# Performance work log

Hardware: AMD Instinct MI355X
Metric: run time of the kernel (lower is better)

The kernel has to match this reference:

```python
import jax, jax.numpy as jnp
import numpy as np

N, C, D, K = 8192, 1024, 256, 20
N_WAYS = 20
REC_OUT = 7 * 7 * 256  # 12544

def _lrelu(v):
    return jnp.where(v > 0, v, 0.01 * v)  # nn.LeakyReLU default slope

def setup_inputs() -> dict:
    key = jax.random.key(0)
    ks = jax.random.split(key, 16)
    s = lambda shape, k, scale: (jax.random.normal(ks[k], shape, jnp.float32) * scale)
    inp = {
        "x": jax.random.normal(ks[0], (N, C), jnp.float32),
        "prototypes": jax.random.normal(ks[1], (K, D), jnp.float32),
        # sigmas in (0.1, 0.5) as in SigmaScheduler(sigma_min=0.1, sigma_max=0.5)
        "sigmas": 0.1 + 0.4 * jax.random.uniform(ks[2], (K,), jnp.float32),
        "prior": jax.random.uniform(ks[3], (K,), jnp.float32) + 1e-3,
        "W1c": s((C, C), 4, C ** -0.5), "b1c": jnp.zeros((C,), jnp.float32),
        "W2c": s((C, D), 5, C ** -0.5), "b2c": jnp.zeros((D,), jnp.float32),
        "W1b": s((C, C), 6, C ** -0.5), "b1b": jnp.zeros((C,), jnp.float32),
        "W2b": s((C, 4 * (N_WAYS + 1)), 7, C ** -0.5), "b2b": jnp.zeros((4 * (N_WAYS + 1),), jnp.float32),
        "Wr1": s((D, 512), 8, D ** -0.5), "br1": jnp.zeros((512,), jnp.float32),
        "Wr2": s((512, REC_OUT), 9, 512 ** -0.5), "br2": jnp.zeros((REC_OUT,), jnp.float32),
    }
    return inp

def reference(x, prototypes, sigmas, prior,
              W1c, b1c, W2c, b2c,
              W1b, b1b, W2b, b2b,
              Wr1, br1, Wr2, br2):
    # cls_score MLP -> embeddings, L2-normalized
    emb = _lrelu(x @ W1c + b1c) @ W2c + b2c                      # [N, D]
    emb = emb / jnp.linalg.norm(emb, axis=-1, keepdims=True)
    bbox_deltas = _lrelu(x @ W1b + b1b) @ W2b + b2b              # [N, 4*(n_ways+1)]
    # prototypes are unit-normed (randn_normed)
    P = prototypes / jnp.linalg.norm(prototypes, axis=-1, keepdims=True)  # [K, D]
    # squared euclidean distance via dot products (avoids N x K x D intermediate)
    d2 = (jnp.sum(emb * emb, axis=-1, keepdims=True)
          + jnp.sum(P * P, axis=-1)[None, :]
          - 2.0 * (emb @ P.T))                                   # [N, K]
    proba = jnp.exp(-d2 / 2.0 / (sigmas[None, :] ** 2))          # [N, K]
    # priors: softmax(prior / prior.max())
    priors = jax.nn.softmax(prior / jnp.max(prior))
    proba = proba * priors[None, :]
    proba_bg = 1.0 - jnp.max(proba, axis=-1, keepdims=True)      # [N, 1]
    scores = jnp.concatenate([proba_bg, proba], axis=-1)         # [N, K+1]
    # reconstruction MLP
    reconstructions = _lrelu(emb @ Wr1 + br1) @ Wr2 + br2        # [N, 12544]
    return scores, bbox_deltas, emb, reconstructions
```

## Files before the change

### kernel.cpp

```cpp
#include <hip/hip_runtime.h>
#include <hip/hip_bf16.h>

typedef __attribute__((ext_vector_type(8))) __bf16 bf16x8;
typedef __attribute__((ext_vector_type(4))) float f32x4;
typedef __hip_bfloat16 bf16t;

#define DEV __device__ __forceinline__

DEV void async16(const void* g, void* l) {
    __builtin_amdgcn_global_load_lds(
        (const __attribute__((address_space(1))) unsigned int*)g,
        (__attribute__((address_space(3))) unsigned int*)l,
        16, 0, 0);
}

DEV float wave_sum(float s) {
#pragma unroll
    for (int o = 32; o > 0; o >>= 1) s += __shfl_xor(s, o);
    return s;
}

DEV float wave_max(float s) {
#pragma unroll
    for (int o = 32; o > 0; o >>= 1) s = fmaxf(s, __shfl_xor(s, o));
    return s;
}

__global__ void cast_bf16_kernel(const float* __restrict__ in, bf16t* __restrict__ out, int n4) {
    int i = blockIdx.x * blockDim.x + threadIdx.x;
    if (i >= n4) return;
    f32x4 v = *(const f32x4*)(in + (size_t)i * 4);
    bf16t* o = out + (size_t)i * 4;
    o[0] = __float2bfloat16(v.x);
    o[1] = __float2bfloat16(v.y);
    o[2] = __float2bfloat16(v.z);
    o[3] = __float2bfloat16(v.w);
}

__global__ void transpose_bf16_kernel(const float* __restrict__ in, bf16t* __restrict__ out,
                                      int R, int Ccols, int RP) {
    int idx = blockIdx.x * blockDim.x + threadIdx.x;
    if (idx >= RP * R) return;
    int n = idx / R;
    int k = idx - n * R;
    float v = (n < Ccols) ? in[(size_t)k * Ccols + n] : 0.0f;
    out[idx] = __float2bfloat16(v);
}

template <bool LRELU, bool OUTF32, bool NGUARD>
__global__ __launch_bounds__(256) void gemm_bt(
    const bf16t* __restrict__ A, const bf16t* __restrict__ BT,
    const float* __restrict__ bias,
    float* __restrict__ Cf, bf16t* __restrict__ Cb,
    int M, int N, int K) {
    __shared__ __align__(16) char ldsA[8192];
    __shared__ __align__(16) char ldsB[8192];

    const int tid = threadIdx.x;
    const int lane = tid & 63;
    const int w = tid >> 6;
    const int wr = w >> 1, wc = w & 1;
    const int brow = blockIdx.y * 128;
    const int bcol = blockIdx.x * 128;

    f32x4 acc[4][4] = {};

    const int q0 = tid, q1 = tid + 256;
    const int r0 = q0 >> 2, c0 = q0 & 3;
    const int r1 = q1 >> 2, c1 = q1 & 3;
    const int ka0 = ((c0 ^ ((r0 >> 1) & 3)) << 3);
    const int ka1 = ((c1 ^ ((r1 >> 1) & 3)) << 3);

    const bf16t* aSrc0 = A + (size_t)(brow + r0) * K + ka0;
    const bf16t* aSrc1 = A + (size_t)(brow + r1) * K + ka1;
    const bf16t* bSrc0 = BT + (size_t)(bcol + r0) * K + ka0;
    const bf16t* bSrc1 = BT + (size_t)(bcol + r1) * K + ka1;
    char* ldA0 = ldsA + w * 1024;
    char* ldA1 = ldsA + 4096 + w * 1024;
    char* ldB0 = ldsB + w * 1024;
    char* ldB1 = ldsB + 4096 + w * 1024;

    const int j = lane >> 4, rl = lane & 15;
    const char* aAddr[4];
    const char* bAddr[4];
#pragma unroll
    for (int mi = 0; mi < 4; ++mi) {
        int row = wr * 64 + mi * 16 + rl;
        aAddr[mi] = ldsA + row * 64 + ((j ^ ((row >> 1) & 3)) << 4);
    }
#pragma unroll
    for (int ni = 0; ni < 4; ++ni) {
        int row = wc * 64 + ni * 16 + rl;
        bAddr[ni] = ldsB + row * 64 + ((j ^ ((row >> 1) & 3)) << 4);
    }

    for (int k0 = 0; k0 < K; k0 += 32) {
        __syncthreads();
        async16(aSrc0 + k0, ldA0);
        async16(aSrc1 + k0, ldA1);
        async16(bSrc0 + k0, ldB0);
        async16(bSrc1 + k0, ldB1);
        __syncthreads();

        bf16x8 af[4], bfr[4];
#pragma unroll
        for (int mi = 0; mi < 4; ++mi) af[mi] = *(const bf16x8*)aAddr[mi];
#pragma unroll
        for (int ni = 0; ni < 4; ++ni) bfr[ni] = *(const bf16x8*)bAddr[ni];
#pragma unroll
        for (int mi = 0; mi < 4; ++mi)
#pragma unroll
            for (int ni = 0; ni < 4; ++ni)
                acc[mi][ni] = __builtin_amdgcn_mfma_f32_16x16x32_bf16(af[mi], bfr[ni], acc[mi][ni], 0, 0, 0);
    }

#pragma unroll
    for (int mi = 0; mi < 4; ++mi) {
#pragma unroll
        for (int ni = 0; ni < 4; ++ni) {
            int col = bcol + wc * 64 + ni * 16 + (lane & 15);
            if (!NGUARD || col < N) {
                float bv = bias[col];
#pragma unroll
                for (int r = 0; r < 4; ++r) {
                    int row = brow + wr * 64 + mi * 16 + (lane >> 4) * 4 + r;
                    float v = acc[mi][ni][r] + bv;
                    if (LRELU) v = v > 0.0f ? v : 0.01f * v;
                    if (OUTF32) Cf[(size_t)row * N + col] = v;
                    else        Cb[(size_t)row * N + col] = __float2bfloat16(v);
                }
            }
        }
    }
}

__global__ void normalize_kernel(const float* __restrict__ raw, float* __restrict__ outf,
                                 bf16t* __restrict__ outb) {
    int row = blockIdx.x * 4 + (threadIdx.x >> 6);
    int lane = threadIdx.x & 63;
    f32x4 v = *(const f32x4*)(raw + (size_t)row * 256 + lane * 4);
    float s = wave_sum(v.x * v.x + v.y * v.y + v.z * v.z + v.w * v.w);
    float rn = 1.0f / sqrtf(s);
    f32x4 o = v * rn;
    *(f32x4*)(outf + (size_t)row * 256 + lane * 4) = o;
    bf16t* ob = outb + (size_t)row * 256 + lane * 4;
    ob[0] = __float2bfloat16(o.x);
    ob[1] = __float2bfloat16(o.y);
    ob[2] = __float2bfloat16(o.z);
    ob[3] = __float2bfloat16(o.w);
}

__global__ void proto_kernel(const float* __restrict__ proto, const float* __restrict__ prior,
                             float* __restrict__ Pn, float* __restrict__ sp, float* __restrict__ priors) {
    int w = threadIdx.x >> 6, lane = threadIdx.x & 63;
    for (int r = w; r < 20; r += 4) {
        f32x4 v = *(const f32x4*)(proto + (size_t)r * 256 + lane * 4);
        float s = wave_sum(v.x * v.x + v.y * v.y + v.z * v.z + v.w * v.w);
        float rn = 1.0f / sqrtf(s);
        f32x4 p = v * rn;
        *(f32x4*)(Pn + (size_t)r * 256 + lane * 4) = p;
        float s2 = wave_sum(p.x * p.x + p.y * p.y + p.z * p.z + p.w * p.w);
        if (lane == 0) sp[r] = s2;
    }
    if (threadIdx.x < 64) {
        float pv = (lane < 20) ? prior[lane] : -1e30f;
        float m = wave_max(pv);
        float e = (lane < 20) ? expf(pv / m) : 0.0f;
        float ssum = wave_sum(e);
        if (lane < 20) priors[lane] = e / ssum;
    }
}

__global__ void scores_kernel(const float* __restrict__ emb, const float* __restrict__ Pn,
                              const float* __restrict__ sp, const float* __restrict__ priors,
                              const float* __restrict__ sig, float* __restrict__ out) {
    int row = blockIdx.x * 4 + (threadIdx.x >> 6);
    int lane = threadIdx.x & 63;
    f32x4 e = *(const f32x4*)(emb + (size_t)row * 256 + lane * 4);
    float se = wave_sum(e.x * e.x + e.y * e.y + e.z * e.z + e.w * e.w);
    float keep = 0.0f, mx = -1.0f;
    for (int k = 0; k < 20; ++k) {
        f32x4 p = *(const f32x4*)(Pn + (size_t)k * 256 + lane * 4);
        float d = wave_sum(e.x * p.x + e.y * p.y + e.z * p.z + e.w * p.w);
        float d2 = se + sp[k] - 2.0f * d;
        float sgv = sig[k];
        float pr = expf(-d2 / (2.0f * sgv * sgv)) * priors[k];
        mx = fmaxf(mx, pr);
        if (lane == k + 1) keep = pr;
    }
    if (lane == 0) keep = 1.0f - mx;
    if (lane < 21) out[(size_t)row * 21 + lane] = keep;
}

extern "C" void kernel_launch(void* const* d_in, const int* in_sizes, int n_in,
                              void* d_out, int out_size, void* d_ws, size_t ws_size,
                              hipStream_t stream) {
    const float* x     = (const float*)d_in[0];
    const float* proto = (const float*)d_in[1];
    const float* sig   = (const float*)d_in[2];
    const float* prior = (const float*)d_in[3];
    const float* W1c = (const float*)d_in[4];
    const float* b1c = (const float*)d_in[5];
    const float* W2c = (const float*)d_in[6];
    const float* b2c = (const float*)d_in[7];
    const float* W1b = (const float*)d_in[8];
    const float* b1b = (const float*)d_in[9];
    const float* W2b = (const float*)d_in[10];
    const float* b2b = (const float*)d_in[11];
    const float* Wr1 = (const float*)d_in[12];
    const float* br1 = (const float*)d_in[13];
    const float* Wr2 = (const float*)d_in[14];
    const float* br2 = (const float*)d_in[15];

    float* out = (float*)d_out;
    float* out_scores = out;
    float* out_bbox   = out + 172032;
    float* out_emb    = out + 860160;
    float* out_rec    = out + 2957312;

    char* ws = (char*)d_ws;
    size_t off = 0;
    auto alloc = [&](size_t b) { char* p = ws + off; off += (b + 255) & ~(size_t)255; return p; };
    bf16t* xb     = (bf16t*)alloc(8192ull * 1024 * 2);
    bf16t* w1ct   = (bf16t*)alloc(1024ull * 1024 * 2);
    bf16t* w1bt   = (bf16t*)alloc(1024ull * 1024 * 2);
    bf16t* w2ct   = (bf16t*)alloc(256ull * 1024 * 2);
    bf16t* w2bt   = (bf16t*)alloc(128ull * 1024 * 2);
    bf16t* wr1t   = (bf16t*)alloc(512ull * 256 * 2);
    bf16t* wr2t   = (bf16t*)alloc(12544ull * 512 * 2);
    bf16t* hc     = (bf16t*)alloc(8192ull * 1024 * 2);
    bf16t* hb     = (bf16t*)alloc(8192ull * 1024 * 2);
    float* embraw = (float*)alloc(8192ull * 256 * 4);
    bf16t* embb   = (bf16t*)alloc(8192ull * 256 * 2);
    bf16t* rech   = (bf16t*)alloc(8192ull * 512 * 2);
    float* Pn     = (float*)alloc(20 * 256 * 4);
    float* spv    = (float*)alloc(20 * 4);
    float* priors = (float*)alloc(20 * 4);
    (void)ws_size; (void)in_sizes; (void)n_in; (void)out_size;

    cast_bf16_kernel<<<8192, 256, 0, stream>>>(x, xb, 8192 * 1024 / 4);
    transpose_bf16_kernel<<<4096, 256, 0, stream>>>(W1c, w1ct, 1024, 1024, 1024);
    transpose_bf16_kernel<<<4096, 256, 0, stream>>>(W1b, w1bt, 1024, 1024, 1024);
    transpose_bf16_kernel<<<1024, 256, 0, stream>>>(W2c, w2ct, 1024, 256, 256);
    transpose_bf16_kernel<<<512, 256, 0, stream>>>(W2b, w2bt, 1024, 84, 128);
    transpose_bf16_kernel<<<512, 256, 0, stream>>>(Wr1, wr1t, 256, 512, 512);
    transpose_bf16_kernel<<<25088, 256, 0, stream>>>(Wr2, wr2t, 512, 12544, 12544);

    gemm_bt<true, false, false><<<dim3(8, 64), 256, 0, stream>>>(xb, w1ct, b1c, nullptr, hc, 8192, 1024, 1024);
    gemm_bt<true, false, false><<<dim3(8, 64), 256, 0, stream>>>(xb, w1bt, b1b, nullptr, hb, 8192, 1024, 1024);
    gemm_bt<false, true, false><<<dim3(2, 64), 256, 0, stream>>>(hc, w2ct, b2c, embraw, nullptr, 8192, 256, 1024);
    gemm_bt<false, true, true><<<dim3(1, 64), 256, 0, stream>>>(hb, w2bt, b2b, out_bbox, nullptr, 8192, 84, 1024);
    normalize_kernel<<<2048, 256, 0, stream>>>(embraw, out_emb, embb);
    proto_kernel<<<1, 256, 0, stream>>>(proto, prior, Pn, spv, priors);
    scores_kernel<<<2048, 256, 0, stream>>>(out_emb, Pn, spv, priors, sig, out_scores);
    gemm_bt<true, false, false><<<dim3(4, 64), 256, 0, stream>>>(embb, wr1t, br1, nullptr, rech, 8192, 512, 256);
    gemm_bt<false, true, false><<<dim3(98, 64), 256, 0, stream>>>(rech, wr2t, br2, out_rec, nullptr, 8192, 12544, 512);
}
```

Baseline: 802.9 us.

## Tile weight transposes, fuse first-layer GEMMs, merge normalize with scores

Replaces the naive strided transpose with a 32x32 LDS-tiled transpose so weight reads and writes are coalesced. Both first-layer GEMMs are merged into one 8192x2048 GEMM with a split bias, and the second-layer GEMMs read their half through a leading-dimension stride. The normalize and scores kernels are fused, and the cast kernel now writes 16-byte vectors. Together these cut launch count and redundant memory traffic, at the cost of extra lda and bias-select arguments in the GEMM.

```diff
diff --git a/kernel.cpp b/kernel.cpp
--- a/kernel.cpp
+++ b/kernel.cpp
@@ -26,31 +26,46 @@
     return s;
 }
 
-__global__ void cast_bf16_kernel(const float* __restrict__ in, bf16t* __restrict__ out, int n4) {
+__global__ void cast_bf16_kernel(const float* __restrict__ in, bf16t* __restrict__ out, int n8) {
     int i = blockIdx.x * blockDim.x + threadIdx.x;
-    if (i >= n4) return;
-    f32x4 v = *(const f32x4*)(in + (size_t)i * 4);
-    bf16t* o = out + (size_t)i * 4;
-    o[0] = __float2bfloat16(v.x);
-    o[1] = __float2bfloat16(v.y);
-    o[2] = __float2bfloat16(v.z);
-    o[3] = __float2bfloat16(v.w);
-}
-
-__global__ void transpose_bf16_kernel(const float* __restrict__ in, bf16t* __restrict__ out,
-                                      int R, int Ccols, int RP) {
-    int idx = blockIdx.x * blockDim.x + threadIdx.x;
-    if (idx >= RP * R) return;
-    int n = idx / R;
-    int k = idx - n * R;
-    float v = (n < Ccols) ? in[(size_t)k * Ccols + n] : 0.0f;
-    out[idx] = __float2bfloat16(v);
+    if (i >= n8) return;
+    f32x4 a = *(const f32x4*)(in + (size_t)i * 8);
+    f32x4 b = *(const f32x4*)(in + (size_t)i * 8 + 4);
+    union { bf16t h[8]; uint4 u; } r;
+    r.h[0] = __float2bfloat16(a.x); r.h[1] = __float2bfloat16(a.y);
+    r.h[2] = __float2bfloat16(a.z); r.h[3] = __float2bfloat16(a.w);
+    r.h[4] = __float2bfloat16(b.x); r.h[5] = __float2bfloat16(b.y);
+    r.h[6] = __float2bfloat16(b.z); r.h[7] = __float2bfloat16(b.w);
+    *(uint4*)(out + (size_t)i * 8) = r.u;
+}
+
+__global__ void transpose_tile_kernel(const float* __restrict__ in, bf16t* __restrict__ out,
+                                      int R, int C, int CP) {
+    __shared__ float tile[32][33];
+    const int nt = blockIdx.x * 32;
+    const int kt = blockIdx.y * 32;
+    const int tx = threadIdx.x & 31;
+    const int ty = threadIdx.x >> 5;
+#pragma unroll
+    for (int i = 0; i < 4; ++i) {
+        int k = kt + ty + i * 8;
+        int n = nt + tx;
+        tile[ty + i * 8][tx] = (k < R && n < C) ? in[(size_t)k * C + n] : 0.0f;
+    }
+    __syncthreads();
+#pragma unroll
+    for (int i = 0; i < 4; ++i) {
+        int n = nt + ty + i * 8;
+        int k = kt + tx;
+        if (n < CP && k < R)
+            out[(size_t)n * R + k] = __float2bfloat16(tile[tx][ty + i * 8]);
+    }
 }
 
 template <bool LRELU, bool OUTF32, bool NGUARD>
 __global__ __launch_bounds__(256) void gemm_bt(
-    const bf16t* __restrict__ A, const bf16t* __restrict__ BT,
-    const float* __restrict__ bias,
+    const bf16t* __restrict__ A, int lda, const bf16t* __restrict__ BT,
+    const float* __restrict__ bias0, const float* __restrict__ bias1, int nsplit,
     float* __restrict__ Cf, bf16t* __restrict__ Cb,
     int M, int N, int K) {
     __shared__ __align__(16) char ldsA[8192];
@@ -71,8 +86,8 @@
     const int ka0 = ((c0 ^ ((r0 >> 1) & 3)) << 3);
     const int ka1 = ((c1 ^ ((r1 >> 1) & 3)) << 3);
 
-    const bf16t* aSrc0 = A + (size_t)(brow + r0) * K + ka0;
-    const bf16t* aSrc1 = A + (size_t)(brow + r1) * K + ka1;
+    const bf16t* aSrc0 = A + (size_t)(brow + r0) * lda + ka0;
+    const bf16t* aSrc1 = A + (size_t)(brow + r1) * lda + ka1;
     const bf16t* bSrc0 = BT + (size_t)(bcol + r0) * K + ka0;
     const bf16t* bSrc1 = BT + (size_t)(bcol + r1) * K + ka1;
     char* ldA0 = ldsA + w * 1024;
@@ -120,7 +135,7 @@
         for (int ni = 0; ni < 4; ++ni) {
             int col = bcol + wc * 64 + ni * 16 + (lane & 15);
             if (!NGUARD || col < N) {
-                float bv = bias[col];
+                float bv = (col < nsplit) ? bias0[col] : bias1[col - nsplit];
 #pragma unroll
                 for (int r = 0; r < 4; ++r) {
                     int row = brow + wr * 64 + mi * 16 + (lane >> 4) * 4 + r;
@@ -132,22 +147,6 @@
             }
         }
     }
-}
-
-__global__ void normalize_kernel(const float* __restrict__ raw, float* __restrict__ outf,
-                                 bf16t* __restrict__ outb) {
-    int row = blockIdx.x * 4 + (threadIdx.x >> 6);
-    int lane = threadIdx.x & 63;
-    f32x4 v = *(const f32x4*)(raw + (size_t)row * 256 + lane * 4);
-    float s = wave_sum(v.x * v.x + v.y * v.y + v.z * v.z + v.w * v.w);
-    float rn = 1.0f / sqrtf(s);
-    f32x4 o = v * rn;
-    *(f32x4*)(outf + (size_t)row * 256 + lane * 4) = o;
-    bf16t* ob = outb + (size_t)row * 256 + lane * 4;
-    ob[0] = __float2bfloat16(o.x);
-    ob[1] = __float2bfloat16(o.y);
-    ob[2] = __float2bfloat16(o.z);
-    ob[3] = __float2bfloat16(o.w);
 }
 
 __global__ void proto_kernel(const float* __restrict__ proto, const float* __restrict__ prior,
@@ -171,13 +170,24 @@
     }
 }
 
-__global__ void scores_kernel(const float* __restrict__ emb, const float* __restrict__ Pn,
-                              const float* __restrict__ sp, const float* __restrict__ priors,
-                              const float* __restrict__ sig, float* __restrict__ out) {
+__global__ void norm_scores_kernel(const float* __restrict__ raw, const float* __restrict__ Pn,
+                                   const float* __restrict__ sp, const float* __restrict__ priors,
+                                   const float* __restrict__ sig,
+                                   float* __restrict__ outf, bf16t* __restrict__ outb,
+                                   float* __restrict__ scores) {
     int row = blockIdx.x * 4 + (threadIdx.x >> 6);
     int lane = threadIdx.x & 63;
-    f32x4 e = *(const f32x4*)(emb + (size_t)row * 256 + lane * 4);
-    float se = wave_sum(e.x * e.x + e.y * e.y + e.z * e.z + e.w * e.w);
+    f32x4 v = *(const f32x4*)(raw + (size_t)row * 256 + lane * 4);
+    float s = wave_sum(v.x * v.x + v.y * v.y + v.z * v.z + v.w * v.w);
+    float rn = 1.0f / sqrtf(s);
+    f32x4 e = v * rn;
+    *(f32x4*)(outf + (size_t)row * 256 + lane * 4) = e;
+    union { bf16t h[4]; uint2 u; } rb;
+    rb.h[0] = __float2bfloat16(e.x); rb.h[1] = __float2bfloat16(e.y);
+    rb.h[2] = __float2bfloat16(e.z); rb.h[3] = __float2bfloat16(e.w);
+    *(uint2*)(outb + (size_t)row * 256 + lane * 4) = rb.u;
+
+    float se = s * rn * rn;
     float keep = 0.0f, mx = -1.0f;
     for (int k = 0; k < 20; ++k) {
         f32x4 p = *(const f32x4*)(Pn + (size_t)k * 256 + lane * 4);
@@ -189,7 +199,7 @@
         if (lane == k + 1) keep = pr;
     }
     if (lane == 0) keep = 1.0f - mx;
-    if (lane < 21) out[(size_t)row * 21 + lane] = keep;
+    if (lane < 21) scores[(size_t)row * 21 + lane] = keep;
 }
 
 extern "C" void kernel_launch(void* const* d_in, const int* in_sizes, int n_in,
@@ -222,14 +232,12 @@
     size_t off = 0;
     auto alloc = [&](size_t b) { char* p = ws + off; off += (b + 255) & ~(size_t)255; return p; };
     bf16t* xb     = (bf16t*)alloc(8192ull * 1024 * 2);
-    bf16t* w1ct   = (bf16t*)alloc(1024ull * 1024 * 2);
-    bf16t* w1bt   = (bf16t*)alloc(1024ull * 1024 * 2);
+    bf16t* w1t    = (bf16t*)alloc(2048ull * 1024 * 2);
     bf16t* w2ct   = (bf16t*)alloc(256ull * 1024 * 2);
     bf16t* w2bt   = (bf16t*)alloc(128ull * 1024 * 2);
     bf16t* wr1t   = (bf16t*)alloc(512ull * 256 * 2);
     bf16t* wr2t   = (bf16t*)alloc(12544ull * 512 * 2);
-    bf16t* hc     = (bf16t*)alloc(8192ull * 1024 * 2);
-    bf16t* hb     = (bf16t*)alloc(8192ull * 1024 * 2);
+    bf16t* hcb    = (bf16t*)alloc(8192ull * 2048 * 2);
     float* embraw = (float*)alloc(8192ull * 256 * 4);
     bf16t* embb   = (bf16t*)alloc(8192ull * 256 * 2);
     bf16t* rech   = (bf16t*)alloc(8192ull * 512 * 2);
@@ -238,21 +246,24 @@
     float* priors = (float*)alloc(20 * 4);
     (void)ws_size; (void)in_sizes; (void)n_in; (void)out_size;
 
-    cast_bf16_kernel<<<8192, 256, 0, stream>>>(x, xb, 8192 * 1024 / 4);
-    transpose_bf16_kernel<<<4096, 256, 0, stream>>>(W1c, w1ct, 1024, 1024, 1024);
-    transpose_bf16_kernel<<<4096, 256, 0, stream>>>(W1b, w1bt, 1024, 1024, 1024);
-    transpose_bf16_kernel<<<1024, 256, 0, stream>>>(W2c, w2ct, 1024, 256, 256);
-    transpose_bf16_kernel<<<512, 256, 0, stream>>>(W2b, w2bt, 1024, 84, 128);
-    transpose_bf16_kernel<<<512, 256, 0, stream>>>(Wr1, wr1t, 256, 512, 512);
-    transpose_bf16_kernel<<<25088, 256, 0, stream>>>(Wr2, wr2t, 512, 12544, 12544);
-
-    gemm_bt<true, false, false><<<dim3(8, 64), 256, 0, stream>>>(xb, w1ct, b1c, nullptr, hc, 8192, 1024, 1024);
-    gemm_bt<true, false, false><<<dim3(8, 64), 256, 0, stream>>>(xb, w1bt, b1b, nullptr, hb, 8192, 1024, 1024);
-    gemm_bt<false, true, false><<<dim3(2, 64), 256, 0, stream>>>(hc, w2ct, b2c, embraw, nullptr, 8192, 256, 1024);
-    gemm_bt<false, true, true><<<dim3(1, 64), 256, 0, stream>>>(hb, w2bt, b2b, out_bbox, nullptr, 8192, 84, 1024);
-    normalize_kernel<<<2048, 256, 0, stream>>>(embraw, out_emb, embb);
+    cast_bf16_kernel<<<4096, 256, 0, stream>>>(x, xb, 8192 * 1024 / 8);
+    transpose_tile_kernel<<<dim3(32, 32), 256, 0, stream>>>(W1c, w1t, 1024, 1024, 1024);
+    transpose_tile_kernel<<<dim3(32, 32), 256, 0, stream>>>(W1b, w1t + 1024ull * 1024, 1024, 1024, 1024);
+    transpose_tile_kernel<<<dim3(8, 32), 256, 0, stream>>>(W2c, w2ct, 1024, 256, 256);
+    transpose_tile_kernel<<<dim3(4, 32), 256, 0, stream>>>(W2b, w2bt, 1024, 84, 128);
+    transpose_tile_kernel<<<dim3(16, 8), 256, 0, stream>>>(Wr1, wr1t, 256, 512, 512);
+    transpose_tile_kernel<<<dim3(392, 16), 256, 0, stream>>>(Wr2, wr2t, 512, 12544, 12544);
     proto_kernel<<<1, 256, 0, stream>>>(proto, prior, Pn, spv, priors);
-    scores_kernel<<<2048, 256, 0, stream>>>(out_emb, Pn, spv, priors, sig, out_scores);
-    gemm_bt<true, false, false><<<dim3(4, 64), 256, 0, stream>>>(embb, wr1t, br1, nullptr, rech, 8192, 512, 256);
-    gemm_bt<false, true, false><<<dim3(98, 64), 256, 0, stream>>>(rech, wr2t, br2, out_rec, nullptr, 8192, 12544, 512);
-}
+
+    gemm_bt<true, false, false><<<dim3(16, 64), 256, 0, stream>>>(
+        xb, 1024, w1t, b1c, b1b, 1024, nullptr, hcb, 8192, 2048, 1024);
+    gemm_bt<false, true, false><<<dim3(2, 64), 256, 0, stream>>>(
+        hcb, 2048, w2ct, b2c, b2c, 256, embraw, nullptr, 8192, 256, 1024);
+    gemm_bt<false, true, true><<<dim3(1, 64), 256, 0, stream>>>(
+        hcb + 1024, 2048, w2bt, b2b, b2b, 128, out_bbox, nullptr, 8192, 84, 1024);
+    norm_scores_kernel<<<2048, 256, 0, stream>>>(embraw, Pn, spv, priors, sig, out_emb, embb, out_scores);
+    gemm_bt<true, false, false><<<dim3(4, 64), 256, 0, stream>>>(
+        embb, 256, wr1t, br1, br1, 512, nullptr, rech, 8192, 512, 256);
+    gemm_bt<false, true, false><<<dim3(98, 64), 256, 0, stream>>>(
+        rech, 512, wr2t, br2, br2, 12544, out_rec, nullptr, 8192, 12544, 512);
+}
```

Result: faster. 763.8 us (-4.9%).
